# Kernel tuning notes

Measured on AMD Instinct MI355X. Metric: run time of the kernel, lower is better.

## Reference

```python
import jax, jax.numpy as jnp
import numpy as np

IN_DIM = 96
HIDDEN = 256
EPS = 1e-6
NEG = -1e10


def setup_inputs() -> dict:
    key = jax.random.key(0)
    ks = jax.random.split(key, 12)
    B, S = 8, 2048
    q = jax.random.normal(ks[0], (B, S, IN_DIM), dtype=jnp.float32)
    k = jax.random.normal(ks[1], (B, S, IN_DIM), dtype=jnp.float32)
    v = jax.random.normal(ks[2], (B, S, IN_DIM), dtype=jnp.float32)
    mask = jax.random.randint(ks[3], (B, S, S), 0, 2, dtype=jnp.int32)
    s = 1.0 / np.sqrt(IN_DIM)
    Wq = jax.random.normal(ks[4], (IN_DIM, HIDDEN), dtype=jnp.float32) * s
    bq = jax.random.normal(ks[5], (HIDDEN,), dtype=jnp.float32) * 0.01
    Wk = jax.random.normal(ks[6], (IN_DIM, HIDDEN), dtype=jnp.float32) * s
    bk = jax.random.normal(ks[7], (HIDDEN,), dtype=jnp.float32) * 0.01
    Wv = jax.random.normal(ks[8], (IN_DIM, HIDDEN), dtype=jnp.float32) * s
    bv = jax.random.normal(ks[9], (HIDDEN,), dtype=jnp.float32) * 0.01
    gamma = jnp.ones((HIDDEN,), dtype=jnp.float32)
    beta = jnp.zeros((HIDDEN,), dtype=jnp.float32)
    return {"query": q, "key": k, "value": v, "mask": mask,
            "Wq": Wq, "bq": bq, "Wk": Wk, "bk": bk, "Wv": Wv, "bv": bv,
            "gamma": gamma, "beta": beta}


def reference(query, key, value, mask, Wq, bq, Wk, bk, Wv, bv, gamma, beta):
    # Linear projections: [B,S,96] @ [96,H] -> [B,S,H]
    q = jnp.einsum('bsf,fh->bsh', query, Wq) + bq
    k = jnp.einsum('bsf,fh->bsh', key, Wk) + bk
    v = jnp.einsum('bsf,fh->bsh', value, Wv) + bv
    # Scaled dot-product scores: [B,S,S]
    score = jnp.einsum('bqh,bkh->bqk', q, k) / jnp.sqrt(jnp.float32(HIDDEN))
    score = jnp.where(mask == 0, jnp.float32(NEG), score)
    attn = jax.nn.softmax(score, axis=-1)
    out = jnp.einsum('bqk,bkh->bqh', attn, v)
    # LayerNorm over last dim, eps=1e-6
    mu = jnp.mean(out, axis=-1, keepdims=True)
    var = jnp.mean(jnp.square(out - mu), axis=-1, keepdims=True)
    normed = (out - mu) * jax.lax.rsqrt(var + EPS)
    return normed * gamma + beta
```

## Files before the change

### kernel.cpp

```cpp
#include <hip/hip_runtime.h>

#define B_   8
#define S_   2048
#define IN_  96
#define H_   256
#define NROW (B_ * S_)

typedef float    f32x4 __attribute__((ext_vector_type(4)));
typedef _Float16 f16x8 __attribute__((ext_vector_type(8)));
typedef int      i32x4 __attribute__((ext_vector_type(4)));

__device__ __forceinline__ unsigned short f2h(float x) {
    return __builtin_bit_cast(unsigned short, (_Float16)x);
}
__device__ __forceinline__ float h2f(unsigned short x) {
    return (float)__builtin_bit_cast(_Float16, x);
}
__device__ __forceinline__ void lds_barrier() {
    asm volatile("s_waitcnt lgkmcnt(0)\n\ts_barrier" ::: "memory");
}

__global__ __launch_bounds__(256) void wconv_kernel(
    const float* __restrict__ Wq, const float* __restrict__ Wk,
    const float* __restrict__ Wv, unsigned short* __restrict__ wt)
{
    const int p  = blockIdx.x >> 3;
    const int h0 = (blockIdx.x & 7) * 32;
    const float* W = (p == 0) ? Wq : (p == 1) ? Wk : Wv;
    unsigned short* dst = wt + (size_t)p * H_ * IN_ + (size_t)h0 * IN_;

    __shared__ unsigned short lds[32][100];
    const int t = threadIdx.x;
    #pragma unroll
    for (int i = 0; i < 12; ++i) {
        int idx = i * 256 + t;
        int f = idx >> 5;
        int hl = idx & 31;
        lds[hl][f] = f2h(W[f * H_ + h0 + hl]);
    }
    __syncthreads();
    #pragma unroll
    for (int j = 0; j < 6; ++j) {
        int e = (j * 256 + t) * 2;
        int hl = e / IN_, f = e % IN_;
        unsigned int pk = (unsigned int)lds[hl][f] |
                          ((unsigned int)lds[hl][f + 1] << 16);
        ((unsigned int*)dst)[j * 256 + t] = pk;
    }
}

__global__ __launch_bounds__(256) void maskpack_kernel(
    const int* __restrict__ mask, unsigned* __restrict__ pm32)
{
    __shared__ unsigned char nib[4][8][64];
    const int wave = threadIdx.x >> 6;
    const int lane = threadIdx.x & 63;
    const int wid  = blockIdx.x * 4 + wave;
    const int r0   = wid * 2;

    const int* m0 = mask + (size_t)r0 * S_ + lane * 4;
    const int* m1 = m0 + S_;
    i32x4 a[8], b[8];
    #pragma unroll
    for (int j = 0; j < 8; ++j)
        a[j] = __builtin_nontemporal_load((const i32x4*)(m0 + j * 256));
    #pragma unroll
    for (int j = 0; j < 8; ++j)
        b[j] = __builtin_nontemporal_load((const i32x4*)(m1 + j * 256));

    #pragma unroll
    for (int j = 0; j < 8; ++j) {
        unsigned n0 = (a[j][0] != 0 ? 1u : 0u) | (a[j][1] != 0 ? 2u : 0u)
                    | (a[j][2] != 0 ? 4u : 0u) | (a[j][3] != 0 ? 8u : 0u);
        unsigned n1 = (b[j][0] != 0 ? 1u : 0u) | (b[j][1] != 0 ? 2u : 0u)
                    | (b[j][2] != 0 ? 4u : 0u) | (b[j][3] != 0 ? 8u : 0u);
        nib[wave][j][lane] = (unsigned char)(n0 | (n1 << 4));
    }
    asm volatile("s_waitcnt lgkmcnt(0)" ::: "memory");

    unsigned long long v = *(const unsigned long long*)
        &nib[wave][lane >> 3][(lane & 7) * 8];
    unsigned long long x0 = v & 0x0F0F0F0F0F0F0F0FULL;
    unsigned long long x1 = (v >> 4) & 0x0F0F0F0F0F0F0F0FULL;
    x0 = (x0 | (x0 >> 4))  & 0x00FF00FF00FF00FFULL;
    x1 = (x1 | (x1 >> 4))  & 0x00FF00FF00FF00FFULL;
    x0 = (x0 | (x0 >> 8))  & 0x0000FFFF0000FFFFULL;
    x1 = (x1 | (x1 >> 8))  & 0x0000FFFF0000FFFFULL;
    x0 = (x0 | (x0 >> 16)) & 0xFFFFFFFFULL;
    x1 = (x1 | (x1 >> 16)) & 0xFFFFFFFFULL;

    pm32[(size_t)r0 * 64 + lane]       = (unsigned)x0;
    pm32[(size_t)(r0 + 1) * 64 + lane] = (unsigned)x1;
}

__global__ __launch_bounds__(256) void proj_kernel3(
    const float* __restrict__ query, const float* __restrict__ key,
    const float* __restrict__ value, const unsigned short* __restrict__ wt,
    const float* __restrict__ bq, const float* __restrict__ bk,
    const float* __restrict__ bv,
    unsigned short* __restrict__ pq, unsigned short* __restrict__ pk,
    unsigned short* __restrict__ pv)
{
    __shared__ unsigned short Xs[3][16][104];

    const int t    = threadIdx.x;
    const int lane = t & 63;
    const int wave = t >> 6;
    const int col  = lane & 15;
    const int quad = lane >> 4;
    const int bi   = blockIdx.x;
    const int s0   = bi * 16;
    const int b    = s0 >> 11;
    const int sl   = s0 & (S_ - 1);

    const float* srcs[3] = { query + (size_t)s0 * IN_,
                             key   + (size_t)s0 * IN_,
                             value + (size_t)s0 * IN_ };
    #pragma unroll
    for (int p = 0; p < 3; ++p) {
        #pragma unroll
        for (int i = 0; i < 2; ++i) {
            int idx = i * 256 + t;
            if (idx < 384) {
                f32x4 x = *(const f32x4*)(srcs[p] + idx * 4);
                int r = idx / 24;
                int f = (idx - r * 24) * 4;
                unsigned long long pkk =
                    (unsigned long long)f2h(x[0])
                  | ((unsigned long long)f2h(x[1]) << 16)
                  | ((unsigned long long)f2h(x[2]) << 32)
                  | ((unsigned long long)f2h(x[3]) << 48);
                *(unsigned long long*)&Xs[p][r][f] = pkk;
            }
        }
    }
    __syncthreads();

    const int hc = wave;
    #pragma unroll
    for (int p = 0; p < 3; ++p) {
        const unsigned short* wbase = wt + (size_t)p * H_ * IN_;
        f16x8 wfr[4][3];
        #pragma unroll
        for (int ht = 0; ht < 4; ++ht)
            #pragma unroll
            for (int kc = 0; kc < 3; ++kc)
                wfr[ht][kc] = *(const f16x8*)(wbase
                    + (size_t)(hc * 64 + ht * 16 + col) * IN_ + kc * 32 + quad * 8);
        f16x8 xfr[3];
        #pragma unroll
        for (int kc = 0; kc < 3; ++kc)
            xfr[kc] = *(const f16x8*)&Xs[p][col][kc * 32 + quad * 8];

        f32x4 acc[4];
        #pragma unroll
        for (int ht = 0; ht < 4; ++ht) acc[ht] = (f32x4)(0.0f);
        #pragma unroll
        for (int kc = 0; kc < 3; ++kc)
            #pragma unroll
            for (int ht = 0; ht < 4; ++ht)
                acc[ht] = (p < 2)
                    ? __builtin_amdgcn_mfma_f32_16x16x32_f16(xfr[kc], wfr[ht][kc], acc[ht], 0, 0, 0)
                    : __builtin_amdgcn_mfma_f32_16x16x32_f16(wfr[ht][kc], xfr[kc], acc[ht], 0, 0, 0);

        if (p < 2) {
            unsigned short* dst  = (p == 0) ? pq : pk;
            const float*    bias = (p == 0) ? bq : bk;
            #pragma unroll
            for (int ht = 0; ht < 4; ++ht) {
                float bh = bias[hc * 64 + ht * 16 + col];
                const int s    = hc * 2 + (ht >> 1);
                const int lq   = ((ht & 1) * 2 + (col >> 3)) * 16;
                const int j    = col & 7;
                #pragma unroll
                for (int r = 0; r < 4; ++r)
                    dst[(size_t)(((bi * 8 + s) * 64 + lq + quad * 4 + r)) * 8 + j]
                        = f2h(acc[ht][r] + bh);
            }
        } else {
            const int kl  = (sl & 63) + col;
            const int c   = sl >> 6;
            const int s2  = kl >> 5;
            const int qv  = (kl >> 3) & 3;
            const int jj  = col & 7;
            #pragma unroll
            for (int ht = 0; ht < 4; ++ht) {
                f32x4 b4 = *(const f32x4*)(bv + hc * 64 + ht * 16 + quad * 4);
                #pragma unroll
                for (int r = 0; r < 4; ++r)
                    pv[(size_t)(((b * 32 + c) * 32 + hc * 8 + ht * 2 + s2) * 64
                                + qv * 16 + quad * 4 + r) * 8 + jj]
                        = f2h(acc[ht][r] + b4[r]);
            }
        }
    }
}

__global__ __launch_bounds__(256, 3) void attn_kernel(
    const unsigned short* __restrict__ pq, const unsigned short* __restrict__ pk,
    const unsigned short* __restrict__ pv, const unsigned long long* __restrict__ pm,
    unsigned short* __restrict__ Opart, float* __restrict__ lpart)
{
    __shared__ __align__(16) unsigned short Qs[2][4096];
    __shared__ unsigned short P[2][32][68];
    __shared__ float lsum[4][32];

    const int tid  = threadIdx.x;
    const int wave = tid >> 6;
    const int lane = tid & 63;
    const int col  = lane & 15;
    const int quad = lane >> 4;

    const int b     = blockIdx.x & 7;
    const int strip = (blockIdx.x >> 3) & 63;
    const int kh    = blockIdx.x >> 9;
    const int q0    = strip << 5;

    {
        const unsigned short* qsrc = pq + (size_t)(b * 128 + strip * 2) * 4096;
        #pragma unroll
        for (int ph = 0; ph < 4; ++ph) {
            int i = ph * 2048 + tid * 8;
            *(f16x8*)&((unsigned short*)Qs)[i] = *(const f16x8*)(qsrc + i);
        }
    }

    f32x4 O[2][4];
    #pragma unroll
    for (int st = 0; st < 2; ++st)
        #pragma unroll
        for (int ht = 0; ht < 4; ++ht) O[st][ht] = (f32x4)(0.0f);
    float l0 = 0.0f, l1 = 0.0f;

    const unsigned short* pkb = pk + (size_t)(b * 128) * 4096 + lane * 8;
    const unsigned short* pvb = pv + (size_t)(b * 32) * 32 * 512
                                   + (size_t)wave * 8 * 512 + lane * 8;

    const unsigned* pm32 = (const unsigned*)pm;
    const int sh = (wave & 1) * 16 + quad * 4;
    const unsigned* mp0 = pm32 + (size_t)(b * S_ + q0 + col) * 64
                        + kh * 32 + (wave >> 1);
    const unsigned* mp1 = mp0 + 16 * 64;

    f16x8 kf[8];
    #pragma unroll
    for (int s = 0; s < 8; ++s)
        kf[s] = *(const f16x8*)(pkb + (size_t)(kh * 64 + wave) * 4096 + s * 512);

    unsigned mw0 = mp0[0];
    unsigned mw1 = mp1[0];

    __syncthreads();

    #pragma unroll 2
    for (int c = 0; c < 16; ++c) {
        const int pb = c & 1;
        const int cn = (c < 15) ? c + 1 : c;
        const int gc = kh * 16 + c;

        const unsigned short* vb = pvb + (size_t)gc * 32 * 512;
        f16x8 vf[4][2];
        #pragma unroll
        for (int ht = 0; ht < 4; ++ht)
            #pragma unroll
            for (int s2 = 0; s2 < 2; ++s2)
                vf[ht][s2] = *(const f16x8*)(vb + (size_t)(ht * 2 + s2) * 512);

        unsigned mn0 = mp0[cn * 2];
        unsigned mn1 = mp1[cn * 2];

        f32x4 St0 = (f32x4)(0.0f), St1 = (f32x4)(0.0f);
        __builtin_amdgcn_s_setprio(1);
        #pragma unroll
        for (int s = 0; s < 8; ++s) {
            f16x8 q0f = *(const f16x8*)&Qs[0][s * 512 + lane * 8];
            f16x8 q1f = *(const f16x8*)&Qs[1][s * 512 + lane * 8];
            St0 = __builtin_amdgcn_mfma_f32_16x16x32_f16(kf[s], q0f, St0, 0, 0, 0);
            St1 = __builtin_amdgcn_mfma_f32_16x16x32_f16(kf[s], q1f, St1, 0, 0, 0);
        }
        __builtin_amdgcn_s_setprio(0);

        {
            const unsigned short* kb = pkb + (size_t)(kh * 64 + cn * 4 + wave) * 4096;
            #pragma unroll
            for (int s = 0; s < 8; ++s)
                kf[s] = *(const f16x8*)(kb + s * 512);
        }

        {
            unsigned bits = mw0 >> sh;
            unsigned long long pk64 = 0;
            #pragma unroll
            for (int r = 0; r < 4; ++r) {
                float e = exp2f(fmaf(St0[r], 0.0901679843f, -8.65617025f));
                float p = ((bits >> r) & 1u) ? e : 0.0f;
                _Float16 ph = (_Float16)p;
                l0 += (float)ph;
                pk64 |= (unsigned long long)__builtin_bit_cast(unsigned short, ph)
                        << (16 * r);
            }
            *(unsigned long long*)&P[pb][col][wave * 16 + quad * 4] = pk64;
        }
        {
            unsigned bits = mw1 >> sh;
            unsigned long long pk64 = 0;
            #pragma unroll
            for (int r = 0; r < 4; ++r) {
                float e = exp2f(fmaf(St1[r], 0.0901679843f, -8.65617025f));
                float p = ((bits >> r) & 1u) ? e : 0.0f;
                _Float16 ph = (_Float16)p;
                l1 += (float)ph;
                pk64 |= (unsigned long long)__builtin_bit_cast(unsigned short, ph)
                        << (16 * r);
            }
            *(unsigned long long*)&P[pb][16 + col][wave * 16 + quad * 4] = pk64;
        }
        mw0 = mn0; mw1 = mn1;

        lds_barrier();

        __builtin_amdgcn_s_setprio(1);
        #pragma unroll
        for (int st = 0; st < 2; ++st) {
            #pragma unroll
            for (int s2 = 0; s2 < 2; ++s2) {
                union { unsigned long long u[2]; f16x8 v; } pu;
                const unsigned short* pr = &P[pb][st * 16 + col][s2 * 32 + quad * 8];
                pu.u[0] = *(const unsigned long long*)pr;
                pu.u[1] = *(const unsigned long long*)(pr + 4);
                f16x8 pf = pu.v;
                #pragma unroll
                for (int ht = 0; ht < 4; ++ht)
                    O[st][ht] = __builtin_amdgcn_mfma_f32_16x16x32_f16(pf, vf[ht][s2], O[st][ht], 0, 0, 0);
            }
        }
        __builtin_amdgcn_s_setprio(0);
    }

    l0 += __shfl_xor(l0, 16); l0 += __shfl_xor(l0, 32);
    l1 += __shfl_xor(l1, 16); l1 += __shfl_xor(l1, 32);
    if (lane < 16) { lsum[wave][lane] = l0; lsum[wave][16 + lane] = l1; }
    __syncthreads();

    if (wave == 0 && lane < 16) {
        #pragma unroll
        for (int st = 0; st < 2; ++st) {
            float lt = lsum[0][st * 16 + lane] + lsum[1][st * 16 + lane]
                     + lsum[2][st * 16 + lane] + lsum[3][st * 16 + lane];
            lpart[(size_t)kh * NROW + b * S_ + q0 + st * 16 + lane] = lt;
        }
    }

    unsigned short* ob = Opart + (size_t)kh * NROW * H_ + (size_t)(b * S_) * H_;
    #pragma unroll
    for (int st = 0; st < 2; ++st)
        #pragma unroll
        for (int ht = 0; ht < 4; ++ht)
            #pragma unroll
            for (int r = 0; r < 4; ++r)
                ob[(size_t)(q0 + st * 16 + quad * 4 + r) * H_
                   + wave * 64 + ht * 16 + col] = f2h(O[st][ht][r]);
}

__global__ __launch_bounds__(256) void merge_ln_kernel(
    const unsigned short* __restrict__ Opart, const float* __restrict__ lpart,
    const float* __restrict__ gamma, const float* __restrict__ beta,
    float* __restrict__ out)
{
    const int row  = blockIdx.x * 4 + (threadIdx.x >> 6);
    const int lane = threadIdx.x & 63;

    float linv = 1.0f / (lpart[row] + lpart[NROW + row]);

    const unsigned short* o0 = Opart + (size_t)row * H_ + lane * 4;
    const unsigned short* o1 = o0 + (size_t)NROW * H_;
    unsigned long long a0 = *(const unsigned long long*)o0;
    unsigned long long a1 = *(const unsigned long long*)o1;

    float vals[4];
    float sum = 0.0f;
    #pragma unroll
    for (int j = 0; j < 4; ++j) {
        vals[j] = (h2f((unsigned short)(a0 >> (16 * j)))
                 + h2f((unsigned short)(a1 >> (16 * j)))) * linv;
        sum += vals[j];
    }
    sum += __shfl_xor(sum, 1);  sum += __shfl_xor(sum, 2);
    sum += __shfl_xor(sum, 4);  sum += __shfl_xor(sum, 8);
    sum += __shfl_xor(sum, 16); sum += __shfl_xor(sum, 32);
    float mu = sum * (1.0f / H_);

    float sq = 0.0f;
    #pragma unroll
    for (int j = 0; j < 4; ++j) {
        float d = vals[j] - mu;
        sq += d * d;
    }
    sq += __shfl_xor(sq, 1);  sq += __shfl_xor(sq, 2);
    sq += __shfl_xor(sq, 4);  sq += __shfl_xor(sq, 8);
    sq += __shfl_xor(sq, 16); sq += __shfl_xor(sq, 32);
    float rstd = rsqrtf(sq * (1.0f / H_) + 1e-6f);

    f32x4 g  = *(const f32x4*)(gamma + lane * 4);
    f32x4 be = *(const f32x4*)(beta  + lane * 4);
    f32x4 o;
    #pragma unroll
    for (int j = 0; j < 4; ++j)
        o[j] = (vals[j] - mu) * rstd * g[j] + be[j];
    *(f32x4*)(out + (size_t)row * H_ + lane * 4) = o;
}

extern "C" void kernel_launch(void* const* d_in, const int* in_sizes, int n_in,
                              void* d_out, int out_size, void* d_ws, size_t ws_size,
                              hipStream_t stream)
{
    const float* query = (const float*)d_in[0];
    const float* key   = (const float*)d_in[1];
    const float* value = (const float*)d_in[2];
    const int*   mask  = (const int*)d_in[3];
    const float* Wq = (const float*)d_in[4];
    const float* bq = (const float*)d_in[5];
    const float* Wk = (const float*)d_in[6];
    const float* bk = (const float*)d_in[7];
    const float* Wv = (const float*)d_in[8];
    const float* bv = (const float*)d_in[9];
    const float* gamma = (const float*)d_in[10];
    const float* beta  = (const float*)d_in[11];
    float* out = (float*)d_out;

    const size_t NQK = (size_t)B_ * S_ * H_;
    unsigned short* pq = (unsigned short*)d_ws;
    unsigned short* pk = pq + NQK;
    unsigned short* pv = pk + NQK;
    unsigned short* wt = pv + NQK;
    unsigned short* Op = wt + (size_t)3 * H_ * IN_;
    float*          lp = (float*)(Op + (size_t)2 * NROW * H_);
    unsigned long long* pm = (unsigned long long*)(lp + 2 * NROW);

    wconv_kernel<<<24, 256, 0, stream>>>(Wq, Wk, Wv, wt);
    maskpack_kernel<<<2048, 256, 0, stream>>>(mask, (unsigned*)pm);
    proj_kernel3<<<B_ * S_ / 16, 256, 0, stream>>>(query, key, value, wt,
                                                   bq, bk, bv, pq, pk, pv);
    attn_kernel<<<B_ * S_ / 32 * 2, 256, 0, stream>>>(pq, pk, pv, pm, Op, lp);
    merge_ln_kernel<<<NROW / 4, 256, 0, stream>>>(Op, lp, gamma, beta, out);
}
```

Before: 313.2 us.

## Split attention keys four ways and stage output stores through LDS

The attention kernel now splits the key dimension into four chunks instead of two. Each block processes 8 key chunks, and the grid doubles to 2048 blocks, which should fill the GPU better and shrink the tail wave. The fp16 partial outputs are first staged in the now-free Q shared buffer and then written as coalesced 16-byte row stores, replacing the scattered 2-byte stores. The merge/LayerNorm kernel reads and sums four partials and four row sums. The cost is twice the partial-output write and read traffic, and a larger workspace that must still fit the allocation.

```diff
diff --git a/kernel.cpp b/kernel.cpp
--- a/kernel.cpp
+++ b/kernel.cpp
@@ -201,7 +201,7 @@
     const unsigned short* __restrict__ pv, const unsigned long long* __restrict__ pm,
     unsigned short* __restrict__ Opart, float* __restrict__ lpart)
 {
-    __shared__ __align__(16) unsigned short Qs[2][4096];
+    __shared__ __align__(16) unsigned short Qs[8192];
     __shared__ unsigned short P[2][32][68];
     __shared__ float lsum[4][32];
 
@@ -221,7 +221,7 @@
         #pragma unroll
         for (int ph = 0; ph < 4; ++ph) {
             int i = ph * 2048 + tid * 8;
-            *(f16x8*)&((unsigned short*)Qs)[i] = *(const f16x8*)(qsrc + i);
+            *(f16x8*)&Qs[i] = *(const f16x8*)(qsrc + i);
         }
     }
 
@@ -239,13 +239,13 @@
     const unsigned* pm32 = (const unsigned*)pm;
     const int sh = (wave & 1) * 16 + quad * 4;
     const unsigned* mp0 = pm32 + (size_t)(b * S_ + q0 + col) * 64
-                        + kh * 32 + (wave >> 1);
+                        + kh * 16 + (wave >> 1);
     const unsigned* mp1 = mp0 + 16 * 64;
 
     f16x8 kf[8];
     #pragma unroll
     for (int s = 0; s < 8; ++s)
-        kf[s] = *(const f16x8*)(pkb + (size_t)(kh * 64 + wave) * 4096 + s * 512);
+        kf[s] = *(const f16x8*)(pkb + (size_t)(kh * 32 + wave) * 4096 + s * 512);
 
     unsigned mw0 = mp0[0];
     unsigned mw1 = mp1[0];
@@ -253,10 +253,10 @@
     __syncthreads();
 
     #pragma unroll 2
-    for (int c = 0; c < 16; ++c) {
+    for (int c = 0; c < 8; ++c) {
         const int pb = c & 1;
-        const int cn = (c < 15) ? c + 1 : c;
-        const int gc = kh * 16 + c;
+        const int cn = (c < 7) ? c + 1 : c;
+        const int gc = kh * 8 + c;
 
         const unsigned short* vb = pvb + (size_t)gc * 32 * 512;
         f16x8 vf[4][2];
@@ -273,15 +273,15 @@
         __builtin_amdgcn_s_setprio(1);
         #pragma unroll
         for (int s = 0; s < 8; ++s) {
-            f16x8 q0f = *(const f16x8*)&Qs[0][s * 512 + lane * 8];
-            f16x8 q1f = *(const f16x8*)&Qs[1][s * 512 + lane * 8];
+            f16x8 q0f = *(const f16x8*)&Qs[s * 512 + lane * 8];
+            f16x8 q1f = *(const f16x8*)&Qs[4096 + s * 512 + lane * 8];
             St0 = __builtin_amdgcn_mfma_f32_16x16x32_f16(kf[s], q0f, St0, 0, 0, 0);
             St1 = __builtin_amdgcn_mfma_f32_16x16x32_f16(kf[s], q1f, St1, 0, 0, 0);
         }
         __builtin_amdgcn_s_setprio(0);
 
         {
-            const unsigned short* kb = pkb + (size_t)(kh * 64 + cn * 4 + wave) * 4096;
+            const unsigned short* kb = pkb + (size_t)(kh * 32 + cn * 4 + wave) * 4096;
             #pragma unroll
             for (int s = 0; s < 8; ++s)
                 kf[s] = *(const f16x8*)(kb + s * 512);
@@ -351,15 +351,25 @@
         }
     }
 
-    unsigned short* ob = Opart + (size_t)kh * NROW * H_ + (size_t)(b * S_) * H_;
+    unsigned short* OT = Qs;
     #pragma unroll
     for (int st = 0; st < 2; ++st)
         #pragma unroll
         for (int ht = 0; ht < 4; ++ht)
             #pragma unroll
             for (int r = 0; r < 4; ++r)
-                ob[(size_t)(q0 + st * 16 + quad * 4 + r) * H_
-                   + wave * 64 + ht * 16 + col] = f2h(O[st][ht][r]);
+                OT[(st * 16 + quad * 4 + r) * 256 + wave * 64 + ht * 16 + col]
+                    = f2h(O[st][ht][r]);
+    __syncthreads();
+
+    unsigned short* ob = Opart + (size_t)kh * NROW * H_
+                       + (size_t)(b * S_ + q0) * H_;
+    const int rrow = tid >> 3;
+    const int hof  = (tid & 7) * 32;
+    #pragma unroll
+    for (int j = 0; j < 4; ++j)
+        *(f16x8*)(ob + (size_t)rrow * H_ + hof + j * 8)
+            = *(const f16x8*)(OT + rrow * 256 + hof + j * 8);
 }
 
 __global__ __launch_bounds__(256) void merge_ln_kernel(
@@ -370,19 +380,23 @@
     const int row  = blockIdx.x * 4 + (threadIdx.x >> 6);
     const int lane = threadIdx.x & 63;
 
-    float linv = 1.0f / (lpart[row] + lpart[NROW + row]);
+    float linv = 1.0f / (lpart[row] + lpart[NROW + row]
+                       + lpart[2 * NROW + row] + lpart[3 * NROW + row]);
 
     const unsigned short* o0 = Opart + (size_t)row * H_ + lane * 4;
-    const unsigned short* o1 = o0 + (size_t)NROW * H_;
     unsigned long long a0 = *(const unsigned long long*)o0;
-    unsigned long long a1 = *(const unsigned long long*)o1;
+    unsigned long long a1 = *(const unsigned long long*)(o0 + (size_t)NROW * H_);
+    unsigned long long a2 = *(const unsigned long long*)(o0 + (size_t)2 * NROW * H_);
+    unsigned long long a3 = *(const unsigned long long*)(o0 + (size_t)3 * NROW * H_);
 
     float vals[4];
     float sum = 0.0f;
     #pragma unroll
     for (int j = 0; j < 4; ++j) {
         vals[j] = (h2f((unsigned short)(a0 >> (16 * j)))
-                 + h2f((unsigned short)(a1 >> (16 * j)))) * linv;
+                 + h2f((unsigned short)(a1 >> (16 * j)))
+                 + h2f((unsigned short)(a2 >> (16 * j)))
+                 + h2f((unsigned short)(a3 >> (16 * j)))) * linv;
         sum += vals[j];
     }
     sum += __shfl_xor(sum, 1);  sum += __shfl_xor(sum, 2);
@@ -434,13 +448,13 @@
     unsigned short* pv = pk + NQK;
     unsigned short* wt = pv + NQK;
     unsigned short* Op = wt + (size_t)3 * H_ * IN_;
-    float*          lp = (float*)(Op + (size_t)2 * NROW * H_);
-    unsigned long long* pm = (unsigned long long*)(lp + 2 * NROW);
+    float*          lp = (float*)(Op + (size_t)4 * NROW * H_);
+    unsigned long long* pm = (unsigned long long*)(lp + 4 * NROW);
 
     wconv_kernel<<<24, 256, 0, stream>>>(Wq, Wk, Wv, wt);
     maskpack_kernel<<<2048, 256, 0, stream>>>(mask, (unsigned*)pm);
     proj_kernel3<<<B_ * S_ / 16, 256, 0, stream>>>(query, key, value, wt,
                                                    bq, bk, bv, pq, pk, pv);
-    attn_kernel<<<B_ * S_ / 32 * 2, 256, 0, stream>>>(pq, pk, pv, pm, Op, lp);
+    attn_kernel<<<B_ * S_ / 32 * 4, 256, 0, stream>>>(pq, pk, pv, pm, Op, lp);
     merge_ln_kernel<<<NROW / 4, 256, 0, stream>>>(Op, lp, gamma, beta, out);
 }
```

After: 316.7 us. Within noise of the previous version (+1.1%).
